# Kernel tuning notes

Hardware: AMD Instinct MI355X
Metric: run time of the kernel (lower is better)

## Reference

```python
import jax, jax.numpy as jnp
import numpy as np

DIM = 1024
HEADS = 16
HEAD_DIM = DIM // HEADS
MLP_DIM = 4096
EPS = 1e-12  # F.normalize eps


def l2_rms(x, g):
    # repo RMSNorm: F.normalize(x, dim=-1) * sqrt(d) * g  (g is a scalar param)
    d = x.shape[-1]
    n = jnp.sqrt(jnp.sum(x * x, axis=-1, keepdims=True))
    return x / jnp.maximum(n, EPS) * (d ** 0.5) * g


def setup_inputs() -> dict:
    key = jax.random.key(0)
    ks = jax.random.split(key, 8)
    B, N = 2, 2048
    s = lambda fan_in: 1.0 / np.sqrt(fan_in)
    return {
        "x": jax.random.normal(ks[0], (B, N, DIM), jnp.float32),
        "w_qkv": jax.random.normal(ks[1], (DIM, 3 * DIM), jnp.float32) * s(DIM),
        "b_qkv": jnp.zeros((3 * DIM,), jnp.float32),
        "w_proj": jax.random.normal(ks[2], (DIM, DIM), jnp.float32) * s(DIM),
        "b_proj": jnp.zeros((DIM,), jnp.float32),
        "g_norm1": jnp.ones((1,), jnp.float32),
        "g_norm2": jnp.ones((1,), jnp.float32),
        "g_qnorm": jnp.ones((1,), jnp.float32),
        "g_knorm": jnp.ones((1,), jnp.float32),
        "w_fc1": jax.random.normal(ks[3], (DIM, MLP_DIM), jnp.float32) * s(DIM),
        "b_fc1": jnp.zeros((MLP_DIM,), jnp.float32),
        "w_fc2": jax.random.normal(ks[4], (MLP_DIM, DIM), jnp.float32) * s(MLP_DIM),
        "b_fc2": jnp.zeros((DIM,), jnp.float32),
    }


def reference(x, w_qkv, b_qkv, w_proj, b_proj, g_norm1, g_norm2,
              g_qnorm, g_knorm, w_fc1, b_fc1, w_fc2, b_fc2):
    B, N, D = x.shape
    # --- attention branch ---
    h = l2_rms(x, g_norm1)
    qkv = h @ w_qkv + b_qkv                      # [B,N,3D]
    qkv = qkv.reshape(B, N, 3, HEADS, HEAD_DIM)
    q, k, v = [jnp.transpose(qkv[:, :, i], (0, 2, 1, 3)) for i in range(3)]  # [B,H,N,d]
    q = l2_rms(q, g_qnorm)
    k = l2_rms(k, g_knorm)
    scale = HEAD_DIM ** -0.5
    scores = jnp.einsum('bhqd,bhkd->bhqk', q * scale, k)   # explicit [B,H,N,N]
    attn = jax.nn.softmax(scores, axis=-1)
    o = jnp.einsum('bhqk,bhkd->bhqd', attn, v)
    o = jnp.transpose(o, (0, 2, 1, 3)).reshape(B, N, D)
    x = x + (o @ w_proj + b_proj)
    # --- MLP branch ---
    h = l2_rms(x, g_norm2)
    h = jax.nn.gelu(h @ w_fc1 + b_fc1, approximate=True)
    x = x + (h @ w_fc2 + b_fc2)
    return x
```

## Files before the change

kernel.cpp:

```cpp
#include <hip/hip_runtime.h>
#include <stdint.h>

#define SEQ_ 2048
#define DIM_ 1024
#define HD_ 64
#define NH_ 16

typedef __bf16 bf16x8 __attribute__((ext_vector_type(8)));
typedef float f32x4 __attribute__((ext_vector_type(4)));
typedef __attribute__((address_space(1))) unsigned int as1_uint;
typedef __attribute__((address_space(3))) unsigned int as3_uint;

__device__ __forceinline__ unsigned short f2bf(float f) {
  unsigned u = __builtin_bit_cast(unsigned, f);
  u += 0x7fffu + ((u >> 16) & 1u);
  return (unsigned short)(u >> 16);
}
__device__ __forceinline__ float bf2f(unsigned short u) {
  return __builtin_bit_cast(float, ((unsigned)u) << 16);
}
__device__ __forceinline__ unsigned pk_bf2(float lo, float hi) {
  return __builtin_amdgcn_perm(__builtin_bit_cast(unsigned, hi),
                               __builtin_bit_cast(unsigned, lo), 0x07060302u);
}

__device__ __forceinline__ void gload_lds16(const void* g, void* l) {
  __builtin_amdgcn_global_load_lds(
      reinterpret_cast<as1_uint*>(reinterpret_cast<uintptr_t>(g)),
      reinterpret_cast<as3_uint*>(
          static_cast<unsigned int>(reinterpret_cast<uintptr_t>(l))),
      16, 0, 0);
}

__global__ __launch_bounds__(256) void transpose_all(
    const float* __restrict__ w_qkv, const float* __restrict__ w_proj,
    const float* __restrict__ w_fc1, const float* __restrict__ w_fc2,
    unsigned short* __restrict__ o_qkv, unsigned short* __restrict__ o_proj,
    unsigned short* __restrict__ o_fc1, unsigned short* __restrict__ o_fc2) {
  int bid = blockIdx.x;
  const float* W; unsigned short* Wt; int K, N;
  if (bid < 3072)      { W = w_qkv;  Wt = o_qkv;  K = 1024; N = 3072; }
  else if (bid < 4096) { W = w_proj; Wt = o_proj; K = 1024; N = 1024; bid -= 3072; }
  else if (bid < 8192) { W = w_fc1;  Wt = o_fc1;  K = 1024; N = 4096; bid -= 4096; }
  else                 { W = w_fc2;  Wt = o_fc2;  K = 4096; N = 1024; bid -= 8192; }
  const int nx = N >> 5;
  const int n0 = (bid % nx) * 32, k0 = (bid / nx) * 32;
  __shared__ float t[32][33];
  const int tx = threadIdx.x & 31, ty = threadIdx.x >> 5;
#pragma unroll
  for (int i = 0; i < 4; i++)
    t[ty + i * 8][tx] = W[(size_t)(k0 + ty + i * 8) * N + n0 + tx];
  __syncthreads();
#pragma unroll
  for (int i = 0; i < 4; i++)
    Wt[(size_t)(n0 + ty + i * 8) * K + k0 + tx] = f2bf(t[tx][ty + i * 8]);
}

__global__ __launch_bounds__(256) void rmsnorm_k(
    const float* __restrict__ x, const float* __restrict__ g,
    unsigned short* __restrict__ out) {
  const int row = blockIdx.x;
  const float4* xr = (const float4*)(x + (size_t)row * DIM_);
  float4 v = xr[threadIdx.x];
  float ss = v.x * v.x + v.y * v.y + v.z * v.z + v.w * v.w;
  ss += __shfl_xor(ss, 1);  ss += __shfl_xor(ss, 2);  ss += __shfl_xor(ss, 4);
  ss += __shfl_xor(ss, 8);  ss += __shfl_xor(ss, 16); ss += __shfl_xor(ss, 32);
  __shared__ float red[4];
  if ((threadIdx.x & 63) == 0) red[threadIdx.x >> 6] = ss;
  __syncthreads();
  float tot = red[0] + red[1] + red[2] + red[3];
  float sc = 32.0f * g[0] / fmaxf(sqrtf(tot), 1e-12f);
  unsigned short* orow = out + (size_t)row * DIM_;
  const int b4 = threadIdx.x * 4;
  orow[b4 + 0] = f2bf(v.x * sc);
  orow[b4 + 1] = f2bf(v.y * sc);
  orow[b4 + 2] = f2bf(v.z * sc);
  orow[b4 + 3] = f2bf(v.w * sc);
}

template <int EPI>
__global__ __launch_bounds__(256, 2) void gemm_bf16(
    const unsigned short* __restrict__ A, const unsigned short* __restrict__ Bt,
    const float* __restrict__ bias, const float* __restrict__ res,
    void* __restrict__ Cout, int M, int N, int K) {
  __shared__ __align__(16) unsigned short As[128 * 32];
  __shared__ __align__(16) unsigned short Bs[128 * 32];
  const int tid = threadIdx.x;
  const int w = tid >> 6, lane = tid & 63;
  const int wm = w >> 1, wn = w & 1;
  const int quad = lane >> 4, l15 = lane & 15;
  const int bn = blockIdx.x, bm = blockIdx.y;
  const int Kchunk = K / gridDim.z;
  const int kbeg = blockIdx.z * Kchunk;

  f32x4 acc[4][4];
#pragma unroll
  for (int i = 0; i < 4; i++)
#pragma unroll
    for (int j = 0; j < 4; j++) acc[i][j] = f32x4{0.f, 0.f, 0.f, 0.f};

  const int r0 = w * 16 + (lane >> 2);
  const int c0 = (lane & 3) * 8;
  const unsigned short* gA0 = A + (size_t)(bm * 128 + r0) * K + kbeg + c0;
  const unsigned short* gA1 = gA0 + (size_t)64 * K;
  const unsigned short* gB0 = Bt + (size_t)(bn * 128 + r0) * K + kbeg + c0;
  const unsigned short* gB1 = gB0 + (size_t)64 * K;
  unsigned short* lA0 = As + w * 512;
  unsigned short* lA1 = As + 2048 + w * 512;
  unsigned short* lB0 = Bs + w * 512;
  unsigned short* lB1 = Bs + 2048 + w * 512;

  for (int kk = 0; kk < Kchunk; kk += 32) {
    gload_lds16(gA0, lA0);
    gload_lds16(gA1, lA1);
    gload_lds16(gB0, lB0);
    gload_lds16(gB1, lB1);
    gA0 += 32; gA1 += 32; gB0 += 32; gB1 += 32;
    __syncthreads();
    bf16x8 af[4], bf[4];
#pragma unroll
    for (int i = 0; i < 4; i++) {
      af[i] = *(const bf16x8*)&As[(wm * 64 + i * 16 + l15) * 32 + quad * 8];
      bf[i] = *(const bf16x8*)&Bs[(wn * 64 + i * 16 + l15) * 32 + quad * 8];
    }
#pragma unroll
    for (int i = 0; i < 4; i++)
#pragma unroll
      for (int j = 0; j < 4; j++)
        acc[i][j] = __builtin_amdgcn_mfma_f32_16x16x32_bf16(af[i], bf[j], acc[i][j], 0, 0, 0);
    __syncthreads();
  }

  const int rowb = bm * 128 + wm * 64;
  const int colb = bn * 128 + wn * 64;
  float* Cz = (float*)Cout + (size_t)blockIdx.z * M * N;
#pragma unroll
  for (int i = 0; i < 4; i++) {
#pragma unroll
    for (int j = 0; j < 4; j++) {
      const int col = colb + j * 16 + l15;
      const float bv = (EPI == 3) ? 0.0f : bias[col];
#pragma unroll
      for (int r = 0; r < 4; r++) {
        const int row = rowb + i * 16 + quad * 4 + r;
        const size_t idx = (size_t)row * N + col;
        float v = acc[i][j][r] + bv;
        if (EPI == 0) {
          ((unsigned short*)Cout)[idx] = f2bf(v);
        } else if (EPI == 1) {
          ((float*)Cout)[idx] = v + res[idx];
        } else if (EPI == 2) {
          float t = tanhf(0.7978845608028654f * (v + 0.044715f * v * v * v));
          ((unsigned short*)Cout)[idx] = f2bf(0.5f * v * (1.0f + t));
        } else {
          Cz[idx] = v;
        }
      }
    }
  }
}

__global__ __launch_bounds__(256) void reduce_splitk(
    const float* __restrict__ part, int S, const float* __restrict__ res,
    const float* __restrict__ bias, float* __restrict__ out, int N, size_t MN) {
  const size_t n4 = MN >> 2;
  const size_t i = (size_t)blockIdx.x * 256 + threadIdx.x;
  if (i >= n4) return;
  float4 a = ((const float4*)res)[i];
  float4 b = ((const float4*)bias)[i % (size_t)(N >> 2)];
  float sx = a.x + b.x, sy = a.y + b.y, sz = a.z + b.z, sw = a.w + b.w;
  for (int z = 0; z < S; z++) {
    float4 p = ((const float4*)part)[z * n4 + i];
    sx += p.x; sy += p.y; sz += p.z; sw += p.w;
  }
  ((float4*)out)[i] = make_float4(sx, sy, sz, sw);
}

__global__ __launch_bounds__(256) void reduce_rms(
    const float* __restrict__ part, int S, const float* __restrict__ res,
    const float* __restrict__ bias, const float* __restrict__ g,
    float* __restrict__ x2, unsigned short* __restrict__ h2) {
  const int row = blockIdx.x;
  const int t = threadIdx.x;
  const size_t base = (size_t)row * DIM_;
  float4 v = ((const float4*)(res + base))[t];
  float4 b = ((const float4*)bias)[t];
  v.x += b.x; v.y += b.y; v.z += b.z; v.w += b.w;
  for (int z = 0; z < S; z++) {
    float4 p = ((const float4*)(part + (size_t)z * SEQ_ * 2 * DIM_ + base))[t];
    v.x += p.x; v.y += p.y; v.z += p.z; v.w += p.w;
  }
  ((float4*)(x2 + base))[t] = v;
  float ss = v.x * v.x + v.y * v.y + v.z * v.z + v.w * v.w;
  ss += __shfl_xor(ss, 1);  ss += __shfl_xor(ss, 2);  ss += __shfl_xor(ss, 4);
  ss += __shfl_xor(ss, 8);  ss += __shfl_xor(ss, 16); ss += __shfl_xor(ss, 32);
  __shared__ float red[4];
  if ((t & 63) == 0) red[t >> 6] = ss;
  __syncthreads();
  const float tot = red[0] + red[1] + red[2] + red[3];
  const float sc = 32.0f * g[0] / fmaxf(sqrtf(tot), 1e-12f);
  unsigned short* orow = h2 + base;
  const int b4 = t * 4;
  orow[b4 + 0] = f2bf(v.x * sc);
  orow[b4 + 1] = f2bf(v.y * sc);
  orow[b4 + 2] = f2bf(v.z * sc);
  orow[b4 + 3] = f2bf(v.w * sc);
}

__global__ __launch_bounds__(256) void qkv_post(
    const unsigned short* __restrict__ qkv, const float* __restrict__ gq,
    const float* __restrict__ gk, unsigned short* __restrict__ Qs,
    unsigned short* __restrict__ Ks, unsigned short* __restrict__ VT) {
  const int item = blockIdx.x * 4 + (threadIdx.x >> 6);
  const int lane = threadIdx.x & 63;
  const int h = item & 15;
  const int rn = item >> 4;
  const int b = rn >> 11, n = rn & 2047;
  const unsigned short* base = qkv + (size_t)rn * 3072 + h * 64;
  const float qv = bf2f(base[lane]);
  const float kv = bf2f(base[1024 + lane]);
  const float vv = bf2f(base[2048 + lane]);
  float sq = qv * qv, sk = kv * kv;
  sq += __shfl_xor(sq, 1);  sk += __shfl_xor(sk, 1);
  sq += __shfl_xor(sq, 2);  sk += __shfl_xor(sk, 2);
  sq += __shfl_xor(sq, 4);  sk += __shfl_xor(sk, 4);
  sq += __shfl_xor(sq, 8);  sk += __shfl_xor(sk, 8);
  sq += __shfl_xor(sq, 16); sk += __shfl_xor(sk, 16);
  sq += __shfl_xor(sq, 32); sk += __shfl_xor(sk, 32);
  const float qs = qv / fmaxf(sqrtf(sq), 1e-12f) * gq[0];
  const float ks = kv / fmaxf(sqrtf(sk), 1e-12f) * (8.0f * gk[0]);
  const int bh = b * 16 + h;
  Qs[((size_t)bh * SEQ_ + n) * HD_ + lane] = f2bf(qs);
  Ks[((size_t)bh * SEQ_ + n) * HD_ + lane] = f2bf(ks);
  VT[((size_t)bh * HD_ + lane) * SEQ_ + n] = f2bf(vv);
}

#define PLD_ 72
__global__ __launch_bounds__(256) void attn_fwd(
    const unsigned short* __restrict__ Qs, const unsigned short* __restrict__ Ks,
    const unsigned short* __restrict__ VT, const float* __restrict__ gq,
    const float* __restrict__ gk, unsigned short* __restrict__ O) {
  __shared__ __align__(16) unsigned short Kl[2][2][64][32];
  __shared__ __align__(16) unsigned short Vl[2][2][64][32];
  __shared__ __align__(16) unsigned short Pl[4][16 * PLD_];
  const int bh = blockIdx.x, qt = blockIdx.y;
  const int w = threadIdx.x >> 6, lane = threadIdx.x & 63;
  const int quad = lane >> 4, l15 = lane & 15;
  const float M = 8.0f * fabsf(gq[0] * gk[0]);
  const unsigned short* Qb = Qs + (size_t)bh * SEQ_ * HD_;
  const unsigned short* Kb = Ks + (size_t)bh * SEQ_ * HD_;
  const unsigned short* Vb = VT + (size_t)bh * HD_ * SEQ_;
  const int q0 = qt * 64 + w * 16;
  const bf16x8 qa0 = *(const bf16x8*)&Qb[(q0 + l15) * HD_ + quad * 8];
  const bf16x8 qa1 = *(const bf16x8*)&Qb[(q0 + l15) * HD_ + 32 + quad * 8];

  const unsigned short* gsrc[4];
  unsigned short* ldst[2][4];
  int gstep[4];
#pragma unroll
  for (int i = 0; i < 4; i++) {
    const int idx = w * 4 + i;
    if (idx < 8) {
      const int kc = idx >> 2, kh = idx & 3;
      ldst[0][i] = &Kl[0][kc][kh * 16][0];
      ldst[1][i] = &Kl[1][kc][kh * 16][0];
      gsrc[i] = &Kb[(size_t)(kh * 16 + (lane >> 2)) * HD_ + kc * 32 + (lane & 3) * 8];
      gstep[i] = 64 * HD_;
    } else {
      const int j = idx - 8;
      const int kc = j >> 2, dh = j & 3;
      ldst[0][i] = &Vl[0][kc][dh * 16][0];
      ldst[1][i] = &Vl[1][kc][dh * 16][0];
      gsrc[i] = &Vb[(size_t)(dh * 16 + (lane >> 2)) * SEQ_ + kc * 32 + (lane & 3) * 8];
      gstep[i] = 64;
    }
  }

  f32x4 o[4];
  float lacc = 0.0f;
#pragma unroll
  for (int c = 0; c < 4; c++) o[c] = f32x4{0.f, 0.f, 0.f, 0.f};
  unsigned short* Pw = &Pl[w][0];

#pragma unroll
  for (int i = 0; i < 4; i++) {
    gload_lds16(gsrc[i], ldst[0][i]);
    gsrc[i] += gstep[i];
  }

  for (int kt = 0; kt < SEQ_ / 64; kt++) {
    const int cb = kt & 1;
    __syncthreads();
    if (kt + 1 < SEQ_ / 64) {
#pragma unroll
      for (int i = 0; i < 4; i++) {
        gload_lds16(gsrc[i], ldst[(kt + 1) & 1][i]);
        gsrc[i] += gstep[i];
      }
    }
    f32x4 st[4];
#pragma unroll
    for (int kn = 0; kn < 4; kn++) {
      const bf16x8 kf0 = *(const bf16x8*)&Kl[cb][0][kn * 16 + l15][quad * 8];
      const bf16x8 kf1 = *(const bf16x8*)&Kl[cb][1][kn * 16 + l15][quad * 8];
      st[kn] = __builtin_amdgcn_mfma_f32_16x16x32_bf16(kf0, qa0, f32x4{0.f, 0.f, 0.f, 0.f}, 0, 0, 0);
      st[kn] = __builtin_amdgcn_mfma_f32_16x16x32_bf16(kf1, qa1, st[kn], 0, 0, 0);
    }
#pragma unroll
    for (int kn = 0; kn < 4; kn++) {
      const float p0 = __expf(st[kn][0] - M);
      const float p1 = __expf(st[kn][1] - M);
      const float p2 = __expf(st[kn][2] - M);
      const float p3 = __expf(st[kn][3] - M);
      lacc += (p0 + p1) + (p2 + p3);
      uint2 pk;
      pk.x = pk_bf2(p0, p1);
      pk.y = pk_bf2(p2, p3);
      *(uint2*)&Pw[l15 * PLD_ + kn * 16 + quad * 4] = pk;
    }
    asm volatile("s_waitcnt lgkmcnt(0)" ::: "memory");
    const bf16x8 pa0 = *(const bf16x8*)&Pw[l15 * PLD_ + quad * 8];
    const bf16x8 pa1 = *(const bf16x8*)&Pw[l15 * PLD_ + 32 + quad * 8];
#pragma unroll
    for (int c = 0; c < 4; c++) {
      const bf16x8 vf0 = *(const bf16x8*)&Vl[cb][0][c * 16 + l15][quad * 8];
      const bf16x8 vf1 = *(const bf16x8*)&Vl[cb][1][c * 16 + l15][quad * 8];
      o[c] = __builtin_amdgcn_mfma_f32_16x16x32_bf16(pa0, vf0, o[c], 0, 0, 0);
      o[c] = __builtin_amdgcn_mfma_f32_16x16x32_bf16(pa1, vf1, o[c], 0, 0, 0);
    }
  }

  lacc += __shfl_xor(lacc, 16);
  lacc += __shfl_xor(lacc, 32);
  const float linv = 1.0f / lacc;
  float lr[4];
#pragma unroll
  for (int r = 0; r < 4; r++) lr[r] = __shfl(linv, quad * 4 + r);
  const int b = bh >> 4, h = bh & 15;
#pragma unroll
  for (int c = 0; c < 4; c++)
#pragma unroll
    for (int r = 0; r < 4; r++) {
      const int row = q0 + quad * 4 + r;
      O[((size_t)(b * SEQ_ + row)) * DIM_ + h * 64 + c * 16 + l15] =
          f2bf(o[c][r] * lr[r]);
    }
}

extern "C" void kernel_launch(void* const* d_in, const int* in_sizes, int n_in,
                              void* d_out, int out_size, void* d_ws, size_t ws_size,
                              hipStream_t stream) {
  const float* x      = (const float*)d_in[0];
  const float* w_qkv  = (const float*)d_in[1];
  const float* b_qkv  = (const float*)d_in[2];
  const float* w_proj = (const float*)d_in[3];
  const float* b_proj = (const float*)d_in[4];
  const float* g1     = (const float*)d_in[5];
  const float* g2     = (const float*)d_in[6];
  const float* gq     = (const float*)d_in[7];
  const float* gk     = (const float*)d_in[8];
  const float* w_fc1  = (const float*)d_in[9];
  const float* b_fc1  = (const float*)d_in[10];
  const float* w_fc2  = (const float*)d_in[11];
  const float* b_fc2  = (const float*)d_in[12];
  float* out = (float*)d_out;

  char* p = (char*)d_ws;
  auto alloc = [&](size_t bytes) {
    char* r = p;
    p += (bytes + 255) & ~(size_t)255;
    return r;
  };
  const size_t MB = 1ull << 20;
  unsigned short* wqkvT  = (unsigned short*)alloc(3072ull * 1024 * 2);
  unsigned short* wprojT = (unsigned short*)alloc(1024ull * 1024 * 2);
  unsigned short* wfc1T  = (unsigned short*)alloc(4096ull * 1024 * 2);
  unsigned short* wfc2T  = (unsigned short*)alloc(1024ull * 4096 * 2);
  unsigned short* h1     = (unsigned short*)alloc(4096ull * 1024 * 2);
  unsigned short* QsB = (unsigned short*)alloc(32ull * SEQ_ * HD_ * 2);
  unsigned short* KsB = (unsigned short*)alloc(32ull * SEQ_ * HD_ * 2);
  unsigned short* VTB = (unsigned short*)alloc(32ull * SEQ_ * HD_ * 2);
  float* x2 = (float*)alloc(4096ull * 1024 * 4);
  unsigned short* h2 = (unsigned short*)alloc(4096ull * 1024 * 2);
  char* big = p;
  const size_t rem = ws_size - (size_t)(p - (char*)d_ws);
  unsigned short* qkvb = (unsigned short*)big;
  unsigned short* h3   = (unsigned short*)big;
  float* proj_part = (float*)big;
  float* fc2_part  = (float*)(big + 32 * MB);
  const int S_pr  = rem >= 64 * MB ? 2 : 1;
  const int S_fc2 = rem >= 96 * MB ? 4 : (rem >= 64 * MB ? 2 : 1);
  unsigned short* Obuf = h1;
  const size_t MN = 4096ull * 1024;

  transpose_all<<<12288, 256, 0, stream>>>(w_qkv, w_proj, w_fc1, w_fc2,
                                           wqkvT, wprojT, wfc1T, wfc2T);
  rmsnorm_k<<<4096, 256, 0, stream>>>(x, g1, h1);
  gemm_bf16<0><<<dim3(3072 / 128, 4096 / 128), 256, 0, stream>>>(
      h1, wqkvT, b_qkv, nullptr, qkvb, 4096, 3072, 1024);
  qkv_post<<<16384, 256, 0, stream>>>(qkvb, gq, gk, QsB, KsB, VTB);
  attn_fwd<<<dim3(32, 32), 256, 0, stream>>>(QsB, KsB, VTB, gq, gk, Obuf);
  if (S_pr > 1) {
    gemm_bf16<3><<<dim3(1024 / 128, 4096 / 128, S_pr), 256, 0, stream>>>(
        Obuf, wprojT, b_proj, nullptr, proj_part, 4096, 1024, 1024);
    reduce_rms<<<4096, 256, 0, stream>>>(proj_part, S_pr, x, b_proj, g2, x2, h2);
  } else {
    gemm_bf16<1><<<dim3(1024 / 128, 4096 / 128), 256, 0, stream>>>(
        Obuf, wprojT, b_proj, x, x2, 4096, 1024, 1024);
    rmsnorm_k<<<4096, 256, 0, stream>>>(x2, g2, h2);
  }
  gemm_bf16<2><<<dim3(4096 / 128, 4096 / 128), 256, 0, stream>>>(
      h2, wfc1T, b_fc1, nullptr, h3, 4096, 4096, 1024);
  if (S_fc2 > 1) {
    gemm_bf16<3><<<dim3(1024 / 128, 4096 / 128, S_fc2), 256, 0, stream>>>(
        h3, wfc2T, b_fc2, nullptr, fc2_part, 4096, 1024, 4096);
    reduce_splitk<<<(MN / 4 + 255) / 256, 256, 0, stream>>>(
        fc2_part, S_fc2, x2, b_fc2, out, 1024, MN);
  } else {
    gemm_bf16<1><<<dim3(1024 / 128, 4096 / 128), 256, 0, stream>>>(
        h3, wfc2T, b_fc2, x2, out, 4096, 1024, 4096);
  }
}
```

Measured before the change: 420.3 us.

## Split attention over key chunks with merge kernel, use exp2, drop LDS double buffer

Attention is split along the key dimension into SA partitions via a third grid axis, so more workgroups run and each handles a share of the keys. Each partition writes unnormalised fp32 outputs and row sums, and a new merge kernel adds them and normalises to bf16. The log2(e) factor is folded into Q so the softmax can use the native exp2. The K/V LDS double buffering is replaced by single-buffered loads with a sync before and after each tile, which exposes load latency, and the fp32 partials add memory traffic and an extra launch.

```diff
diff --git a/kernel.cpp b/kernel.cpp
--- a/kernel.cpp
+++ b/kernel.cpp
@@ -10,6 +10,12 @@
 typedef float f32x4 __attribute__((ext_vector_type(4)));
 typedef __attribute__((address_space(1))) unsigned int as1_uint;
 typedef __attribute__((address_space(3))) unsigned int as3_uint;
+
+#if __has_builtin(__builtin_amdgcn_exp2f)
+#define EXP2(x) __builtin_amdgcn_exp2f(x)
+#else
+#define EXP2(x) exp2f(x)
+#endif
 
 __device__ __forceinline__ unsigned short f2bf(float f) {
   unsigned u = __builtin_bit_cast(unsigned, f);
@@ -227,7 +233,7 @@
   sq += __shfl_xor(sq, 8);  sk += __shfl_xor(sk, 8);
   sq += __shfl_xor(sq, 16); sk += __shfl_xor(sk, 16);
   sq += __shfl_xor(sq, 32); sk += __shfl_xor(sk, 32);
-  const float qs = qv / fmaxf(sqrtf(sq), 1e-12f) * gq[0];
+  const float qs = qv / fmaxf(sqrtf(sq), 1e-12f) * (1.4426950408889634f * gq[0]);
   const float ks = kv / fmaxf(sqrtf(sk), 1e-12f) * (8.0f * gk[0]);
   const int bh = b * 16 + h;
   Qs[((size_t)bh * SEQ_ + n) * HD_ + lane] = f2bf(qs);
@@ -239,39 +245,41 @@
 __global__ __launch_bounds__(256) void attn_fwd(
     const unsigned short* __restrict__ Qs, const unsigned short* __restrict__ Ks,
     const unsigned short* __restrict__ VT, const float* __restrict__ gq,
-    const float* __restrict__ gk, unsigned short* __restrict__ O) {
-  __shared__ __align__(16) unsigned short Kl[2][2][64][32];
-  __shared__ __align__(16) unsigned short Vl[2][2][64][32];
+    const float* __restrict__ gk, float* __restrict__ o_part,
+    float* __restrict__ l_part) {
+  __shared__ __align__(16) unsigned short Kl[2][64][32];
+  __shared__ __align__(16) unsigned short Vl[2][64][32];
   __shared__ __align__(16) unsigned short Pl[4][16 * PLD_];
-  const int bh = blockIdx.x, qt = blockIdx.y;
+  const int bh = blockIdx.x, qt = blockIdx.y, kv = blockIdx.z;
+  const int Z = gridDim.z;
+  const int nkt = SEQ_ / 64 / Z;
   const int w = threadIdx.x >> 6, lane = threadIdx.x & 63;
   const int quad = lane >> 4, l15 = lane & 15;
-  const float M = 8.0f * fabsf(gq[0] * gk[0]);
+  const float M = 8.0f * 1.4426950408889634f * fabsf(gq[0] * gk[0]);
   const unsigned short* Qb = Qs + (size_t)bh * SEQ_ * HD_;
   const unsigned short* Kb = Ks + (size_t)bh * SEQ_ * HD_;
   const unsigned short* Vb = VT + (size_t)bh * HD_ * SEQ_;
+  const int key0 = kv * nkt * 64;
   const int q0 = qt * 64 + w * 16;
   const bf16x8 qa0 = *(const bf16x8*)&Qb[(q0 + l15) * HD_ + quad * 8];
   const bf16x8 qa1 = *(const bf16x8*)&Qb[(q0 + l15) * HD_ + 32 + quad * 8];
 
   const unsigned short* gsrc[4];
-  unsigned short* ldst[2][4];
+  unsigned short* ldst[4];
   int gstep[4];
 #pragma unroll
   for (int i = 0; i < 4; i++) {
     const int idx = w * 4 + i;
     if (idx < 8) {
       const int kc = idx >> 2, kh = idx & 3;
-      ldst[0][i] = &Kl[0][kc][kh * 16][0];
-      ldst[1][i] = &Kl[1][kc][kh * 16][0];
-      gsrc[i] = &Kb[(size_t)(kh * 16 + (lane >> 2)) * HD_ + kc * 32 + (lane & 3) * 8];
+      ldst[i] = &Kl[kc][kh * 16][0];
+      gsrc[i] = &Kb[(size_t)(key0 + kh * 16 + (lane >> 2)) * HD_ + kc * 32 + (lane & 3) * 8];
       gstep[i] = 64 * HD_;
     } else {
       const int j = idx - 8;
       const int kc = j >> 2, dh = j & 3;
-      ldst[0][i] = &Vl[0][kc][dh * 16][0];
-      ldst[1][i] = &Vl[1][kc][dh * 16][0];
-      gsrc[i] = &Vb[(size_t)(dh * 16 + (lane >> 2)) * SEQ_ + kc * 32 + (lane & 3) * 8];
+      ldst[i] = &Vl[kc][dh * 16][0];
+      gsrc[i] = &Vb[(size_t)(dh * 16 + (lane >> 2)) * SEQ_ + key0 + kc * 32 + (lane & 3) * 8];
       gstep[i] = 64;
     }
   }
@@ -282,36 +290,27 @@
   for (int c = 0; c < 4; c++) o[c] = f32x4{0.f, 0.f, 0.f, 0.f};
   unsigned short* Pw = &Pl[w][0];
 
-#pragma unroll
-  for (int i = 0; i < 4; i++) {
-    gload_lds16(gsrc[i], ldst[0][i]);
-    gsrc[i] += gstep[i];
-  }
-
-  for (int kt = 0; kt < SEQ_ / 64; kt++) {
-    const int cb = kt & 1;
+  for (int kt = 0; kt < nkt; kt++) {
+#pragma unroll
+    for (int i = 0; i < 4; i++) {
+      gload_lds16(gsrc[i], ldst[i]);
+      gsrc[i] += gstep[i];
+    }
     __syncthreads();
-    if (kt + 1 < SEQ_ / 64) {
-#pragma unroll
-      for (int i = 0; i < 4; i++) {
-        gload_lds16(gsrc[i], ldst[(kt + 1) & 1][i]);
-        gsrc[i] += gstep[i];
-      }
-    }
     f32x4 st[4];
 #pragma unroll
     for (int kn = 0; kn < 4; kn++) {
-      const bf16x8 kf0 = *(const bf16x8*)&Kl[cb][0][kn * 16 + l15][quad * 8];
-      const bf16x8 kf1 = *(const bf16x8*)&Kl[cb][1][kn * 16 + l15][quad * 8];
+      const bf16x8 kf0 = *(const bf16x8*)&Kl[0][kn * 16 + l15][quad * 8];
+      const bf16x8 kf1 = *(const bf16x8*)&Kl[1][kn * 16 + l15][quad * 8];
       st[kn] = __builtin_amdgcn_mfma_f32_16x16x32_bf16(kf0, qa0, f32x4{0.f, 0.f, 0.f, 0.f}, 0, 0, 0);
       st[kn] = __builtin_amdgcn_mfma_f32_16x16x32_bf16(kf1, qa1, st[kn], 0, 0, 0);
     }
 #pragma unroll
     for (int kn = 0; kn < 4; kn++) {
-      const float p0 = __expf(st[kn][0] - M);
-      const float p1 = __expf(st[kn][1] - M);
-      const float p2 = __expf(st[kn][2] - M);
-      const float p3 = __expf(st[kn][3] - M);
+      const float p0 = EXP2(st[kn][0] - M);
+      const float p1 = EXP2(st[kn][1] - M);
+      const float p2 = EXP2(st[kn][2] - M);
+      const float p3 = EXP2(st[kn][3] - M);
       lacc += (p0 + p1) + (p2 + p3);
       uint2 pk;
       pk.x = pk_bf2(p0, p1);
@@ -323,28 +322,50 @@
     const bf16x8 pa1 = *(const bf16x8*)&Pw[l15 * PLD_ + 32 + quad * 8];
 #pragma unroll
     for (int c = 0; c < 4; c++) {
-      const bf16x8 vf0 = *(const bf16x8*)&Vl[cb][0][c * 16 + l15][quad * 8];
-      const bf16x8 vf1 = *(const bf16x8*)&Vl[cb][1][c * 16 + l15][quad * 8];
+      const bf16x8 vf0 = *(const bf16x8*)&Vl[0][c * 16 + l15][quad * 8];
+      const bf16x8 vf1 = *(const bf16x8*)&Vl[1][c * 16 + l15][quad * 8];
       o[c] = __builtin_amdgcn_mfma_f32_16x16x32_bf16(pa0, vf0, o[c], 0, 0, 0);
       o[c] = __builtin_amdgcn_mfma_f32_16x16x32_bf16(pa1, vf1, o[c], 0, 0, 0);
     }
+    __syncthreads();
   }
 
   lacc += __shfl_xor(lacc, 16);
   lacc += __shfl_xor(lacc, 32);
-  const float linv = 1.0f / lacc;
-  float lr[4];
-#pragma unroll
-  for (int r = 0; r < 4; r++) lr[r] = __shfl(linv, quad * 4 + r);
   const int b = bh >> 4, h = bh & 15;
+  if (quad == 0)
+    l_part[(size_t)kv * 32 * SEQ_ + bh * SEQ_ + qt * 64 + w * 16 + l15] = lacc;
+  float* ob = o_part + (size_t)kv * 2 * SEQ_ * DIM_;
 #pragma unroll
   for (int c = 0; c < 4; c++)
 #pragma unroll
     for (int r = 0; r < 4; r++) {
       const int row = q0 + quad * 4 + r;
-      O[((size_t)(b * SEQ_ + row)) * DIM_ + h * 64 + c * 16 + l15] =
-          f2bf(o[c][r] * lr[r]);
-    }
+      ob[((size_t)(b * SEQ_ + row)) * DIM_ + h * 64 + c * 16 + l15] = o[c][r];
+    }
+}
+
+__global__ __launch_bounds__(256) void attn_merge(
+    const float* __restrict__ o_part, const float* __restrict__ l_part, int S,
+    unsigned short* __restrict__ Obuf) {
+  const int rn = blockIdx.x;
+  const int b = rn >> 11, n = rn & 2047;
+  const int t = threadIdx.x;
+  const int col0 = t * 4;
+  const int h = col0 >> 6;
+  const int bh = b * 16 + h;
+  float4 v = ((const float4*)(o_part + (size_t)rn * DIM_))[t];
+  float l = l_part[bh * SEQ_ + n];
+  for (int z = 1; z < S; z++) {
+    float4 p = ((const float4*)(o_part + (size_t)z * 2 * SEQ_ * DIM_ + (size_t)rn * DIM_))[t];
+    v.x += p.x; v.y += p.y; v.z += p.z; v.w += p.w;
+    l += l_part[(size_t)z * 32 * SEQ_ + bh * SEQ_ + n];
+  }
+  const float inv = 1.0f / l;
+  uint2 pk;
+  pk.x = pk_bf2(v.x * inv, v.y * inv);
+  pk.y = pk_bf2(v.z * inv, v.w * inv);
+  *(uint2*)&Obuf[(size_t)rn * DIM_ + col0] = pk;
 }
 
 extern "C" void kernel_launch(void* const* d_in, const int* in_sizes, int n_in,
@@ -390,6 +411,9 @@
   float* fc2_part  = (float*)(big + 32 * MB);
   const int S_pr  = rem >= 64 * MB ? 2 : 1;
   const int S_fc2 = rem >= 96 * MB ? 4 : (rem >= 64 * MB ? 2 : 1);
+  const int SA = rem >= 33 * MB ? 2 : 1;
+  float* o_part = (float*)big;
+  float* l_part = (float*)(big + (size_t)SA * 16 * MB);
   unsigned short* Obuf = h1;
   const size_t MN = 4096ull * 1024;
 
@@ -399,7 +423,9 @@
   gemm_bf16<0><<<dim3(3072 / 128, 4096 / 128), 256, 0, stream>>>(
       h1, wqkvT, b_qkv, nullptr, qkvb, 4096, 3072, 1024);
   qkv_post<<<16384, 256, 0, stream>>>(qkvb, gq, gk, QsB, KsB, VTB);
-  attn_fwd<<<dim3(32, 32), 256, 0, stream>>>(QsB, KsB, VTB, gq, gk, Obuf);
+  attn_fwd<<<dim3(32, 32, SA), 256, 0, stream>>>(QsB, KsB, VTB, gq, gk,
+                                                 o_part, l_part);
+  attn_merge<<<4096, 256, 0, stream>>>(o_part, l_part, SA, Obuf);
   if (S_pr > 1) {
     gemm_bf16<3><<<dim3(1024 / 128, 4096 / 128, S_pr), 256, 0, stream>>>(
         Obuf, wprojT, b_proj, nullptr, proj_part, 4096, 1024, 1024);
```

Result: no change. 416.8 us (-0.8%).

## Load K/V fragments directly from global into registers, drop LDS staging

Applied to the files above, without the earlier changes.

The attention kernel no longer stages K and V tiles through shared memory with global_load_lds and per-tile barriers. Each wave now loads its MFMA fragments straight from global (L2) into registers, with register-level prefetch of the next K tile. The grid is transposed so consecutive blocks share the same head, which favours L2 reuse. The softmax uses native exp2 with log2(e) folded into the Q scale and the max constant. The trade-off is that all four waves now fetch the same K/V separately, raising L2 traffic and register pressure in exchange for removing the barriers.

```diff
diff --git a/kernel.cpp b/kernel.cpp
--- a/kernel.cpp
+++ b/kernel.cpp
@@ -10,6 +10,12 @@
 typedef float f32x4 __attribute__((ext_vector_type(4)));
 typedef __attribute__((address_space(1))) unsigned int as1_uint;
 typedef __attribute__((address_space(3))) unsigned int as3_uint;
+
+#if __has_builtin(__builtin_amdgcn_exp2f)
+#define EXP2(x) __builtin_amdgcn_exp2f(x)
+#else
+#define EXP2(x) exp2f(x)
+#endif
 
 __device__ __forceinline__ unsigned short f2bf(float f) {
   unsigned u = __builtin_bit_cast(unsigned, f);
@@ -227,7 +233,7 @@
   sq += __shfl_xor(sq, 8);  sk += __shfl_xor(sk, 8);
   sq += __shfl_xor(sq, 16); sk += __shfl_xor(sk, 16);
   sq += __shfl_xor(sq, 32); sk += __shfl_xor(sk, 32);
-  const float qs = qv / fmaxf(sqrtf(sq), 1e-12f) * gq[0];
+  const float qs = qv / fmaxf(sqrtf(sq), 1e-12f) * (1.4426950408889634f * gq[0]);
   const float ks = kv / fmaxf(sqrtf(sk), 1e-12f) * (8.0f * gk[0]);
   const int bh = b * 16 + h;
   Qs[((size_t)bh * SEQ_ + n) * HD_ + lane] = f2bf(qs);
@@ -240,13 +246,11 @@
     const unsigned short* __restrict__ Qs, const unsigned short* __restrict__ Ks,
     const unsigned short* __restrict__ VT, const float* __restrict__ gq,
     const float* __restrict__ gk, unsigned short* __restrict__ O) {
-  __shared__ __align__(16) unsigned short Kl[2][2][64][32];
-  __shared__ __align__(16) unsigned short Vl[2][2][64][32];
   __shared__ __align__(16) unsigned short Pl[4][16 * PLD_];
-  const int bh = blockIdx.x, qt = blockIdx.y;
+  const int qt = blockIdx.x, bh = blockIdx.y;
   const int w = threadIdx.x >> 6, lane = threadIdx.x & 63;
   const int quad = lane >> 4, l15 = lane & 15;
-  const float M = 8.0f * fabsf(gq[0] * gk[0]);
+  const float M = 8.0f * 1.4426950408889634f * fabsf(gq[0] * gk[0]);
   const unsigned short* Qb = Qs + (size_t)bh * SEQ_ * HD_;
   const unsigned short* Kb = Ks + (size_t)bh * SEQ_ * HD_;
   const unsigned short* Vb = VT + (size_t)bh * HD_ * SEQ_;
@@ -254,79 +258,60 @@
   const bf16x8 qa0 = *(const bf16x8*)&Qb[(q0 + l15) * HD_ + quad * 8];
   const bf16x8 qa1 = *(const bf16x8*)&Qb[(q0 + l15) * HD_ + 32 + quad * 8];
 
-  const unsigned short* gsrc[4];
-  unsigned short* ldst[2][4];
-  int gstep[4];
-#pragma unroll
-  for (int i = 0; i < 4; i++) {
-    const int idx = w * 4 + i;
-    if (idx < 8) {
-      const int kc = idx >> 2, kh = idx & 3;
-      ldst[0][i] = &Kl[0][kc][kh * 16][0];
-      ldst[1][i] = &Kl[1][kc][kh * 16][0];
-      gsrc[i] = &Kb[(size_t)(kh * 16 + (lane >> 2)) * HD_ + kc * 32 + (lane & 3) * 8];
-      gstep[i] = 64 * HD_;
-    } else {
-      const int j = idx - 8;
-      const int kc = j >> 2, dh = j & 3;
-      ldst[0][i] = &Vl[0][kc][dh * 16][0];
-      ldst[1][i] = &Vl[1][kc][dh * 16][0];
-      gsrc[i] = &Vb[(size_t)(dh * 16 + (lane >> 2)) * SEQ_ + kc * 32 + (lane & 3) * 8];
-      gstep[i] = 64;
-    }
-  }
-
   f32x4 o[4];
   float lacc = 0.0f;
 #pragma unroll
   for (int c = 0; c < 4; c++) o[c] = f32x4{0.f, 0.f, 0.f, 0.f};
   unsigned short* Pw = &Pl[w][0];
 
-#pragma unroll
-  for (int i = 0; i < 4; i++) {
-    gload_lds16(gsrc[i], ldst[0][i]);
-    gsrc[i] += gstep[i];
+  bf16x8 kf0[4], kf1[4];
+#pragma unroll
+  for (int kn = 0; kn < 4; kn++) {
+    kf0[kn] = *(const bf16x8*)&Kb[(size_t)(kn * 16 + l15) * HD_ + quad * 8];
+    kf1[kn] = *(const bf16x8*)&Kb[(size_t)(kn * 16 + l15) * HD_ + 32 + quad * 8];
   }
 
   for (int kt = 0; kt < SEQ_ / 64; kt++) {
-    const int cb = kt & 1;
-    __syncthreads();
-    if (kt + 1 < SEQ_ / 64) {
-#pragma unroll
-      for (int i = 0; i < 4; i++) {
-        gload_lds16(gsrc[i], ldst[(kt + 1) & 1][i]);
-        gsrc[i] += gstep[i];
-      }
-    }
+    const int n0 = kt * 64;
     f32x4 st[4];
 #pragma unroll
     for (int kn = 0; kn < 4; kn++) {
-      const bf16x8 kf0 = *(const bf16x8*)&Kl[cb][0][kn * 16 + l15][quad * 8];
-      const bf16x8 kf1 = *(const bf16x8*)&Kl[cb][1][kn * 16 + l15][quad * 8];
-      st[kn] = __builtin_amdgcn_mfma_f32_16x16x32_bf16(kf0, qa0, f32x4{0.f, 0.f, 0.f, 0.f}, 0, 0, 0);
-      st[kn] = __builtin_amdgcn_mfma_f32_16x16x32_bf16(kf1, qa1, st[kn], 0, 0, 0);
+      st[kn] = __builtin_amdgcn_mfma_f32_16x16x32_bf16(kf0[kn], qa0, f32x4{0.f, 0.f, 0.f, 0.f}, 0, 0, 0);
+      st[kn] = __builtin_amdgcn_mfma_f32_16x16x32_bf16(kf1[kn], qa1, st[kn], 0, 0, 0);
+    }
+    bf16x8 vf0[4], vf1[4];
+#pragma unroll
+    for (int c = 0; c < 4; c++) {
+      vf0[c] = *(const bf16x8*)&Vb[(size_t)(c * 16 + l15) * SEQ_ + n0 + quad * 8];
+      vf1[c] = *(const bf16x8*)&Vb[(size_t)(c * 16 + l15) * SEQ_ + n0 + 32 + quad * 8];
     }
 #pragma unroll
     for (int kn = 0; kn < 4; kn++) {
-      const float p0 = __expf(st[kn][0] - M);
-      const float p1 = __expf(st[kn][1] - M);
-      const float p2 = __expf(st[kn][2] - M);
-      const float p3 = __expf(st[kn][3] - M);
+      const float p0 = EXP2(st[kn][0] - M);
+      const float p1 = EXP2(st[kn][1] - M);
+      const float p2 = EXP2(st[kn][2] - M);
+      const float p3 = EXP2(st[kn][3] - M);
       lacc += (p0 + p1) + (p2 + p3);
       uint2 pk;
       pk.x = pk_bf2(p0, p1);
       pk.y = pk_bf2(p2, p3);
       *(uint2*)&Pw[l15 * PLD_ + kn * 16 + quad * 4] = pk;
     }
+    if (kt + 1 < SEQ_ / 64) {
+      const int n1 = n0 + 64;
+#pragma unroll
+      for (int kn = 0; kn < 4; kn++) {
+        kf0[kn] = *(const bf16x8*)&Kb[(size_t)(n1 + kn * 16 + l15) * HD_ + quad * 8];
+        kf1[kn] = *(const bf16x8*)&Kb[(size_t)(n1 + kn * 16 + l15) * HD_ + 32 + quad * 8];
+      }
+    }
     asm volatile("s_waitcnt lgkmcnt(0)" ::: "memory");
     const bf16x8 pa0 = *(const bf16x8*)&Pw[l15 * PLD_ + quad * 8];
     const bf16x8 pa1 = *(const bf16x8*)&Pw[l15 * PLD_ + 32 + quad * 8];
 #pragma unroll
     for (int c = 0; c < 4; c++) {
-      const bf16x8 vf0 = *(const bf16x8*)&Vl[cb][0][c * 16 + l15][quad * 8];
-      const bf16x8 vf1 = *(const bf16x8*)&Vl[cb][1][c * 16 + l15][quad * 8];
-      o[c] = __builtin_amdgcn_mfma_f32_16x16x32_bf16(pa0, vf0, o[c], 0, 0, 0);
-      o[c] = __builtin_amdgcn_mfma_f32_16x16x32_bf16(pa1, vf1, o[c], 0, 0, 0);
+      o[c] = __builtin_amdgcn_mfma_f32_16x16x32_bf16(pa0, vf0[c], o[c], 0, 0, 0);
+      o[c] = __builtin_amdgcn_mfma_f32_16x16x32_bf16(pa1, vf1[c], o[c], 0, 0, 0);
     }
   }
 
```

Result: slower. 570.7 us (+35.8%).
